# Kernel tuning notes

Measured on AMD Instinct MI355X. Metric: run time of the kernel, lower is better.

Reference implementation:

```python
import jax, jax.numpy as jnp
import numpy as np

NUM_CLASSES = 8
INNER = 2048
BETA = 1.0


def _pairwise_dist(x):
    # ||x_i - x_j||_2 via Gram identity; safe sqrt so grads are finite on the zero diagonal.
    sq = jnp.sum(x * x, axis=-1)
    d2 = jnp.maximum(sq[:, None] + sq[None, :] - 2.0 * (x @ x.T), 0.0)
    safe = jnp.where(d2 > 0, d2, 1.0)
    return jnp.where(d2 > 0, jnp.sqrt(safe), 0.0)


def _mst_edges(dist):
    # Prim's algorithm on a dense [n, n] distance matrix -> (n-1) MST edges.
    # These edges are exactly the death times of 0d persistent homology features.
    n = dist.shape[0]
    big = jnp.finfo(dist.dtype).max
    in_tree = jnp.zeros((n,), bool).at[0].set(True)
    mind = dist[0]                      # best distance from tree to each vertex
    parent = jnp.zeros((n,), jnp.int32)  # tree vertex realizing that distance

    def step(carry, _):
        in_tree, mind, parent = carry
        j = jnp.argmin(jnp.where(in_tree, big, mind)).astype(jnp.int32)
        edge = (parent[j], j)
        in_tree = in_tree.at[j].set(True)
        dj = dist[j]
        upd = dj < mind
        mind = jnp.where(upd, dj, mind)
        parent = jnp.where(upd, j, parent)
        return (in_tree, mind, parent), edge

    _, (e0, e1) = jax.lax.scan(step, (in_tree, mind, parent), None, length=n - 1)
    return e0, e1


def setup_inputs() -> dict:
    key = jax.random.key(0)
    features = jax.random.normal(key, (NUM_CLASSES * INNER, 64), dtype=jnp.float32)
    return {"features": features}


def reference(features):
    feats = features.reshape(NUM_CLASSES, INNER, -1)  # per-class slices

    def per_class(x):
        dist = _pairwise_dist(x)
        e0, e1 = _mst_edges(jax.lax.stop_gradient(dist))  # edge selection has zero gradient
        edge_len = dist[e0, e1]                            # gather MST edge lengths
        return jnp.mean(jnp.abs(edge_len - BETA))          # mean_absolute_error vs beta

    return jnp.sum(jax.vmap(per_class)(feats))  # loss accumulated over classes
```

## Files before the change

### kernel.cpp

```cpp
#include <hip/hip_runtime.h>

#define NCLS 8
#define NPT  2048
#define DIM  64
#define NROUNDS 11
#define NBLK 512
#define CBLK 64
#define FINF 3.402823466e38f
#define INFK 0xFFFFFFFFu
#define INF64 0xFFFFFFFFFFFFFFFFull

#define CTR_FIN      256
#define CTR_FALLBACK 257
#define NCNT         (CTR_FALLBACK + NROUNDS * NCLS)

typedef unsigned int u32;
typedef unsigned long long u64;
typedef unsigned short u16;
typedef _Float16 f16_t;
typedef __attribute__((ext_vector_type(8))) f16_t f16x8;
typedef __attribute__((ext_vector_type(4))) float f32x4;
typedef __attribute__((ext_vector_type(4))) u32 u32x4;

#define MFMAH(a, b, c) __builtin_amdgcn_mfma_f32_16x16x32_f16((a), (b), (c), 0, 0, 0)

#define ALOAD_U64(p) __hip_atomic_load((p), __ATOMIC_RELAXED, __HIP_MEMORY_SCOPE_AGENT)
#define ALOAD_U32(p) __hip_atomic_load((p), __ATOMIC_RELAXED, __HIP_MEMORY_SCOPE_AGENT)
#define ALOAD_F32(p) __hip_atomic_load((p), __ATOMIC_RELAXED, __HIP_MEMORY_SCOPE_AGENT)
#define ASTORE_F32(p, v) __hip_atomic_store((p), (v), __ATOMIC_RELAXED, __HIP_MEMORY_SCOPE_AGENT)

__device__ __forceinline__ void cbar(u32* __restrict__ ctr, int c, int inst) {
    __syncthreads();
    if (threadIdx.x == 0) {
        u32* a = &ctr[c * 32 + inst];
        __hip_atomic_fetch_add(a, 1u, __ATOMIC_RELAXED, __HIP_MEMORY_SCOPE_AGENT);
        while (ALOAD_U32(a) < CBLK) __builtin_amdgcn_s_sleep(1);
    }
    __syncthreads();
}

__global__ void convinit_kernel(const float* __restrict__ x, u16* __restrict__ xh,
                                float* __restrict__ sq, u32* __restrict__ comp,
                                u64* __restrict__ minEdge, float* __restrict__ lossAcc,
                                u32* __restrict__ done, u32* __restrict__ counters) {
    int row  = blockIdx.x * 4 + (threadIdx.x >> 6);
    int lane = threadIdx.x & 63;
    size_t idx = (size_t)row * DIM + lane;
    float v = x[idx];
    xh[idx] = __builtin_bit_cast(u16, (f16_t)v);
    float s = v * v;
    #pragma unroll
    for (int m = 32; m >= 1; m >>= 1) s += __shfl_xor(s, m);
    if (lane == 0) {
        sq[row]   = s;
        comp[row] = (u32)(row & (NPT - 1));
        if (row < NCLS) { lossAcc[row] = 0.0f; done[row] = 0u; }
    }
    int g = blockIdx.x * 256 + threadIdx.x;
    if (g < 2 * NCLS * NPT) minEdge[g] = INF64;
    if (g < NCNT) counters[g] = 0u;
}

__global__ __launch_bounds__(256) void persist2_kernel(
    const u16* __restrict__ xh, const float* __restrict__ sq,
    u64* __restrict__ minEdge, float* __restrict__ lossAcc,
    u32* __restrict__ counters, float* __restrict__ out)
{
    __shared__ u16   compL[NPT];
    __shared__ float sqC[512];
    __shared__ __align__(16) char uni[NPT * 8 + NPT * 2];
    __shared__ float rwS[4];
    __shared__ u32   rcS[4];
    __shared__ u32   shRoot, shConv;

    u64* minT    = (u64*)uni;
    u64* edgeL   = (u64*)uni;
    u16* parentL = (u16*)(uni + NPT * 8);

    const int c    = blockIdx.z;
    const int rb   = blockIdx.y;
    const int cs   = blockIdx.x;
    const int tid  = threadIdx.x;
    const int lane = tid & 63;
    const int w    = tid >> 6;
    const bool leader = (rb == 0 && cs == 0);

    const size_t xbase = (size_t)c * NPT * DIM;
    sqC[tid]       = sq[(size_t)c * NPT + cs * 512 + tid];
    sqC[tid + 256] = sq[(size_t)c * NPT + cs * 512 + 256 + tid];
    #pragma unroll
    for (int k = 0; k < 8; ++k) compL[k * 256 + tid] = (u16)(k * 256 + tid);

    const int kq   = (lane >> 4) * 8;
    const int arow = rb * 128 + w * 32 + (lane & 15);
    f16x8 Ah[2][2];
    #pragma unroll
    for (int rt = 0; rt < 2; ++rt)
        #pragma unroll
        for (int kk = 0; kk < 2; ++kk) {
            size_t off = xbase + (size_t)(arow + rt * 16) * DIM + kk * 32 + kq;
            Ah[rt][kk] = __builtin_bit_cast(f16x8, *(const u32x4*)(xh + off));
        }
    int   rowg_[2][4];
    float sqrow[2][4];
    #pragma unroll
    for (int rt = 0; rt < 2; ++rt)
        #pragma unroll
        for (int r = 0; r < 4; ++r) {
            int rg = rb * 128 + w * 32 + rt * 16 + ((lane >> 4) << 2) + r;
            rowg_[rt][r] = rg;
            sqrow[rt][r] = sq[(size_t)c * NPT + rg];
        }

    float classLoss = 0.0f;
    __syncthreads();

    for (int rnd = 0; rnd < NROUNDS; ++rnd) {
        u64* edgeGb = minEdge + ((size_t)(rnd & 1) * NCLS + c) * NPT;

        #pragma unroll
        for (int k = 0; k < 8; ++k) minT[k * 256 + tid] = INF64;
        __syncthreads();

        u32 crow[2][4];
        #pragma unroll
        for (int rt = 0; rt < 2; ++rt)
            #pragma unroll
            for (int r = 0; r < 4; ++r) crow[rt][r] = compL[rowg_[rt][r]];

        u32 rm[2][4];
        #pragma unroll
        for (int rt = 0; rt < 2; ++rt)
            #pragma unroll
            for (int r = 0; r < 4; ++r) rm[rt][r] = INFK;

        #pragma unroll 2
        for (int ct = 0; ct < 32; ++ct) {
            const int colb = cs * 512 + ct * 16 + (lane & 15);
            f16x8 Bh[2];
            #pragma unroll
            for (int kk = 0; kk < 2; ++kk) {
                size_t off = xbase + (size_t)colb * DIM + kk * 32 + kq;
                Bh[kk] = __builtin_bit_cast(f16x8, *(const u32x4*)(xh + off));
            }
            u32   ccol = compL[colb];
            float sqc_ = sqC[ct * 16 + (lane & 15)];

            #pragma unroll
            for (int rt = 0; rt < 2; ++rt) {
                f32x4 acc = {0.f, 0.f, 0.f, 0.f};
                acc = MFMAH(Ah[rt][0], Bh[0], acc);
                acc = MFMAH(Ah[rt][1], Bh[1], acc);
                #pragma unroll
                for (int r = 0; r < 4; ++r) {
                    float d2 = fmaf(-2.0f, acc[r], sqrow[rt][r] + sqc_);
                    d2 = fmaxf(d2, 0.0f);
                    u32 bk = (__float_as_uint(d2) + 0x400u) & 0xFFFFF800u;
                    u32 k2 = bk | (u32)colb;
                    k2 = (crow[rt][r] == ccol) ? INFK : k2;
                    rm[rt][r] = min(rm[rt][r], k2);
                }
            }
        }

        const u64 tagbits = (u64)(15 - rnd) << 60;
        #pragma unroll
        for (int rt = 0; rt < 2; ++rt)
            #pragma unroll
            for (int r = 0; r < 4; ++r) {
                u32 bv = rm[rt][r];
                #pragma unroll
                for (int m = 8; m >= 1; m >>= 1)
                    bv = min(bv, (u32)__shfl_xor((int)bv, m));
                if ((lane & 15) == 0 && bv != INFK) {
                    int rowg = rowg_[rt][r];
                    int colg = (int)(bv & 0x7FFu);
                    u32 d21  = bv >> 11;
                    int mn = rowg < colg ? rowg : colg;
                    int mx = rowg < colg ? colg : rowg;
                    u64 key = tagbits | ((u64)d21 << 22) | ((u64)mn << 11) | (u64)mx;
                    atomicMin(&minT[crow[rt][r]], key);
                }
            }
        __syncthreads();

        #pragma unroll
        for (int k = 0; k < 8; ++k) {
            int i = k * 256 + tid;
            u64 e = minT[i];
            if (e != INF64) atomicMin(&edgeGb[i], e);
        }

        cbar(counters, c, rnd);

        #pragma unroll
        for (int k = 0; k < 8; ++k) {
            int i = k * 256 + tid;
            edgeL[i]   = ALOAD_U64(&edgeGb[i]);
            parentL[i] = (u16)i;
        }
        __syncthreads();

        const u64 T = (u64)(15 - rnd);
        float myw = 0.0f;
        u32   mycnt = 0;
        #pragma unroll
        for (int k = 0; k < 8; ++k) {
            int L = k * 256 + tid;
            u64 e = edgeL[L];
            if (e != INF64 && (e >> 60) == T) {
                int mn = (int)((e >> 11) & 0x7FF);
                int mx = (int)(e & 0x7FF);
                u32 A = compL[mn], B = compL[mx];
                u32 O = (A == (u32)L) ? B : A;
                bool mutual = (edgeL[O] == e);
                if (!(mutual && (u32)L > O)) {
                    parentL[L] = (u16)O;
                    float d2 = __uint_as_float(((u32)(e >> 22) & 0x1FFFFFu) << 11);
                    myw += fabsf(sqrtf(d2) - 1.0f);
                    ++mycnt;
                }
            }
        }
        __syncthreads();

        #pragma unroll
        for (int k = 0; k < 8; ++k) {
            int L = k * 256 + tid;
            u32 p1 = parentL[L];
            if (p1 != (u32)L && parentL[p1] == (u32)L && (u32)L > p1)
                parentL[L] = (u16)L;
        }
        __syncthreads();

        for (int it = 0; it < 11; ++it) {
            u16 np[8];
            #pragma unroll
            for (int k = 0; k < 8; ++k) {
                int L = k * 256 + tid;
                np[k] = parentL[parentL[L]];
            }
            __syncthreads();
            #pragma unroll
            for (int k = 0; k < 8; ++k) parentL[k * 256 + tid] = np[k];
            __syncthreads();
        }

        u16 nc[8];
        #pragma unroll
        for (int k = 0; k < 8; ++k) nc[k] = parentL[compL[k * 256 + tid]];
        if (tid == 0) { shRoot = nc[0]; shConv = 1; }
        __syncthreads();
        u32 bad = 0;
        #pragma unroll
        for (int k = 0; k < 8; ++k) {
            compL[k * 256 + tid] = nc[k];
            bad |= (u32)(nc[k] != (u16)shRoot);
        }
        if (bad) shConv = 0;

        #pragma unroll
        for (int m = 32; m >= 1; m >>= 1) {
            myw   += __shfl_xor(myw, m);
            mycnt += (u32)__shfl_xor((int)mycnt, m);
        }
        if (lane == 0) { rwS[w] = myw; rcS[w] = mycnt; }
        __syncthreads();

        classLoss += rwS[0] + rwS[1] + rwS[2] + rwS[3];
        u32 rcTot  = rcS[0] + rcS[1] + rcS[2] + rcS[3];
        if (shConv != 0u || rcTot == 0u) break;
    }

    if (leader && tid == 0) ASTORE_F32(&lossAcc[c], classLoss);
    __syncthreads();
    if (leader && tid == 0) {
        u32 t = __hip_atomic_fetch_add(&counters[CTR_FIN], 1u,
                                       __ATOMIC_RELAXED, __HIP_MEMORY_SCOPE_AGENT);
        if (t == NCLS - 1) {
            float s = 0.0f;
            for (int cc = 0; cc < NCLS; ++cc) s += ALOAD_F32(&lossAcc[cc]);
            out[0] = s * (1.0f / (float)(NPT - 1));
        }
    }
}

__global__ __launch_bounds__(256) void scanmerge_kernel(
    const u16* __restrict__ xh, const float* __restrict__ sq,
    u32* __restrict__ comp, u64* __restrict__ minEdge,
    float* __restrict__ lossAcc, u32* __restrict__ classDone,
    u32* __restrict__ counters, int rnd)
{
    const int c = blockIdx.z;
    if (classDone[c]) return;
    const int cs   = blockIdx.x;
    const int rb   = blockIdx.y;
    const int tid  = threadIdx.x;
    const int lane = tid & 63;
    const int w    = tid >> 6;

    __shared__ u32 compL[NPT];
    __shared__ __align__(16) char bufA[NPT * 4];
    __shared__ __align__(16) char bufB[NPT * 8];
    __shared__ float rw[256];
    __shared__ u32   rc[256];
    __shared__ u32   shTicket;
    __shared__ int   conv;

    float* sqL  = (float*)bufA;
    u64*   minT = (u64*)bufB;

    const u32*   compG = comp + (size_t)c * NPT;
    const float* sqG   = sq + (size_t)c * NPT;
    u64*         edgeG = minEdge + (size_t)c * NPT;

    #pragma unroll
    for (int k = 0; k < NPT / 256; ++k) {
        int i = k * 256 + tid;
        compL[i] = compG[i];
        sqL[i]   = sqG[i];
        minT[i]  = INF64;
    }
    __syncthreads();

    const size_t xbase = (size_t)c * NPT * DIM;
    const int    kq    = (lane >> 4) * 8;
    const int    arow  = rb * 128 + w * 32 + (lane & 15);

    f16x8 Ah[2][2];
    #pragma unroll
    for (int rt = 0; rt < 2; ++rt)
        #pragma unroll
        for (int kk = 0; kk < 2; ++kk) {
            size_t off = xbase + (size_t)(arow + rt * 16) * DIM + kk * 32 + kq;
            Ah[rt][kk] = __builtin_bit_cast(f16x8, *(const u32x4*)(xh + off));
        }

    int   rowg_[2][4];
    float sqrow[2][4];
    u32   crow[2][4];
    #pragma unroll
    for (int rt = 0; rt < 2; ++rt)
        #pragma unroll
        for (int r = 0; r < 4; ++r) {
            int rg = rb * 128 + w * 32 + rt * 16 + ((lane >> 4) << 2) + r;
            rowg_[rt][r] = rg;
            sqrow[rt][r] = sqL[rg];
            crow[rt][r]  = compL[rg];
        }

    u32 rm[2][4];
    #pragma unroll
    for (int rt = 0; rt < 2; ++rt)
        #pragma unroll
        for (int r = 0; r < 4; ++r) rm[rt][r] = INFK;

    #pragma unroll 2
    for (int ct = 0; ct < 32; ++ct) {
        const int colb = cs * 512 + ct * 16 + (lane & 15);
        f16x8 Bh[2];
        #pragma unroll
        for (int kk = 0; kk < 2; ++kk) {
            size_t off = xbase + (size_t)colb * DIM + kk * 32 + kq;
            Bh[kk] = __builtin_bit_cast(f16x8, *(const u32x4*)(xh + off));
        }
        u32   ccol = compL[colb];
        float sqc_ = sqL[colb];

        #pragma unroll
        for (int rt = 0; rt < 2; ++rt) {
            f32x4 acc = {0.f, 0.f, 0.f, 0.f};
            acc = MFMAH(Ah[rt][0], Bh[0], acc);
            acc = MFMAH(Ah[rt][1], Bh[1], acc);
            #pragma unroll
            for (int r = 0; r < 4; ++r) {
                float d2 = fmaf(-2.0f, acc[r], sqrow[rt][r] + sqc_);
                d2 = fmaxf(d2, 0.0f);
                u32 bk = (__float_as_uint(d2) + 0x400u) & 0xFFFFF800u;
                u32 k2 = bk | (u32)colb;
                k2 = (crow[rt][r] == ccol) ? INFK : k2;
                rm[rt][r] = min(rm[rt][r], k2);
            }
        }
    }

    #pragma unroll
    for (int rt = 0; rt < 2; ++rt)
        #pragma unroll
        for (int r = 0; r < 4; ++r) {
            u32 bv = rm[rt][r];
            #pragma unroll
            for (int m = 8; m >= 1; m >>= 1)
                bv = min(bv, (u32)__shfl_xor((int)bv, m));
            if ((lane & 15) == 0 && bv != INFK) {
                int rowg = rowg_[rt][r];
                int colg = (int)(bv & 0x7FFu);
                u32 d21  = bv >> 11;
                int mn = rowg < colg ? rowg : colg;
                int mx = rowg < colg ? colg : rowg;
                u64 key = ((u64)d21 << 22) | ((u64)mn << 11) | (u64)mx;
                atomicMin(&minT[crow[rt][r]], key);
            }
        }
    __syncthreads();

    #pragma unroll
    for (int k = 0; k < NPT / 256; ++k) {
        int i = k * 256 + tid;
        u64 e = minT[i];
        if (e != INF64) atomicMin(&edgeG[i], e);
    }

    __syncthreads();
    if (tid == 0)
        shTicket = __hip_atomic_fetch_add(&counters[CTR_FALLBACK + rnd * NCLS + c], 1u,
                                          __ATOMIC_RELAXED, __HIP_MEMORY_SCOPE_AGENT);
    __syncthreads();
    if (shTicket != 63u) return;

    u32* parentL = (u32*)bufA;
    u64* edgeL   = (u64*)bufB;
    u32* compGm  = comp + (size_t)c * NPT;

    #pragma unroll
    for (int k = 0; k < NPT / 256; ++k) {
        int i = k * 256 + tid;
        edgeL[i]   = ALOAD_U64(&edgeG[i]);
        parentL[i] = (u32)i;
    }
    if (tid == 0) conv = 1;
    __syncthreads();

    float myw = 0.0f;
    int   mycnt = 0;
    #pragma unroll
    for (int k = 0; k < NPT / 256; ++k) {
        int L = k * 256 + tid;
        u64 e = edgeL[L];
        if (e != INF64) {
            int mn = (int)((e >> 11) & 0x7FF);
            int mx = (int)(e & 0x7FF);
            u32 A = compL[mn], B = compL[mx];
            u32 O = (A == (u32)L) ? B : A;
            bool mutual = (edgeL[O] == e);
            if (!(mutual && (u32)L > O)) {
                parentL[L] = O;
                float d2 = __uint_as_float((u32)(e >> 22) << 11);
                myw += fabsf(sqrtf(d2) - 1.0f);
                mycnt += 1;
            }
        }
    }
    __syncthreads();

    #pragma unroll
    for (int k = 0; k < NPT / 256; ++k) {
        int L = k * 256 + tid;
        u32 p1 = parentL[L];
        if (p1 != (u32)L && parentL[p1] == (u32)L && (u32)L > p1) parentL[L] = (u32)L;
    }
    __syncthreads();

    for (int it = 0; it < 11; ++it) {
        u32 np[NPT / 256];
        #pragma unroll
        for (int k = 0; k < NPT / 256; ++k) {
            int L = k * 256 + tid;
            np[k] = parentL[parentL[L]];
        }
        __syncthreads();
        #pragma unroll
        for (int k = 0; k < NPT / 256; ++k) parentL[k * 256 + tid] = np[k];
        __syncthreads();
    }

    u32 root0 = parentL[compL[0]];
    #pragma unroll
    for (int k = 0; k < NPT / 256; ++k) {
        int v = k * 256 + tid;
        u32 nc = parentL[compL[v]];
        compGm[v] = nc;
        if (nc != root0) conv = 0;
        edgeG[v] = INF64;
    }

    rw[tid] = myw; rc[tid] = (u32)mycnt;
    __syncthreads();
    for (int s = 128; s >= 1; s >>= 1) {
        if (tid < s) { rw[tid] += rw[tid + s]; rc[tid] += rc[tid + s]; }
        __syncthreads();
    }
    if (tid == 0) {
        lossAcc[c] += rw[0];
        if (conv || rc[0] == 0u) classDone[c] = 1u;
    }
}

__global__ void final2_kernel(const float* __restrict__ lossAcc, float* __restrict__ out) {
    if (threadIdx.x == 0 && blockIdx.x == 0) {
        float s = 0.0f;
        for (int cc = 0; cc < NCLS; ++cc) s += lossAcc[cc] * (1.0f / (float)(NPT - 1));
        out[0] = s;
    }
}

extern "C" void kernel_launch(void* const* d_in, const int* in_sizes, int n_in,
                              void* d_out, int out_size, void* d_ws, size_t ws_size,
                              hipStream_t stream) {
    const float* x   = (const float*)d_in[0];
    float*       out = (float*)d_out;

    const size_t nv = (size_t)NCLS * NPT;
    const size_t nx = (size_t)NCLS * NPT * DIM;

    const size_t off_me   = 0;
    const size_t off_sq   = off_me + 2 * nv * sizeof(u64);
    const size_t off_comp = off_sq + nv * sizeof(float);
    const size_t off_loss = off_comp + nv * sizeof(u32);
    const size_t off_done = off_loss + NCLS * sizeof(float);
    const size_t off_cnt  = off_done + NCLS * sizeof(u32);
    const size_t off_xh   = off_cnt + (((size_t)NCNT + 7) & ~7ull) * sizeof(u32);
    const size_t need     = off_xh + nx * sizeof(u16);

    if (ws_size < need) return;

    u64*   minEdge  = (u64*)((char*)d_ws + off_me);
    float* sq       = (float*)((char*)d_ws + off_sq);
    u32*   comp     = (u32*)((char*)d_ws + off_comp);
    float* lossAcc  = (float*)((char*)d_ws + off_loss);
    u32*   done     = (u32*)((char*)d_ws + off_done);
    u32*   counters = (u32*)((char*)d_ws + off_cnt);
    u16*   xh       = (u16*)((char*)d_ws + off_xh);

    convinit_kernel<<<(NCLS * NPT) / 4, 256, 0, stream>>>(x, xh, sq, comp,
                                                          minEdge, lossAcc, done,
                                                          counters);

    int dev = 0, cus = 0, maxBlk = 0;
    bool coopOK = (hipGetDevice(&dev) == hipSuccess) &&
                  (hipDeviceGetAttribute(&cus, hipDeviceAttributeMultiprocessorCount,
                                         dev) == hipSuccess) &&
                  (hipOccupancyMaxActiveBlocksPerMultiprocessor(
                       &maxBlk, persist2_kernel, 256, 0) == hipSuccess) &&
                  ((long long)maxBlk * cus >= (long long)NBLK);

    if (coopOK) {
        void* args[] = {(void*)&xh, (void*)&sq, (void*)&minEdge,
                        (void*)&lossAcc, (void*)&counters, (void*)&out};
        hipLaunchCooperativeKernel(reinterpret_cast<void*>(persist2_kernel),
                                   dim3(4, 16, NCLS), dim3(256), args, 0, stream);
    } else {
        for (int r = 0; r < NROUNDS; ++r) {
            scanmerge_kernel<<<dim3(4, NPT / 128, NCLS), 256, 0, stream>>>(
                xh, sq, comp, minEdge, lossAcc, done, counters, r);
        }
        final2_kernel<<<1, 64, 0, stream>>>(lossAcc, out);
    }
}
```

Baseline: 136.1 us.

## Use 512-thread blocks with half the grid and early-exit pointer jumping

The persistent Boruvka kernel now runs with 512-thread blocks covering 256 rows each, which halves the grid to 256 blocks. That means fewer participants in the cross-block barrier and fewer global atomic merges of per-block minima. The pointer-jumping loop now tracks whether any parent changed and exits early once converged, and parentL is widened to u32. The trade is fewer resident blocks relative to CUs, so less parallelism in the distance/MFMA phase, plus an extra barrier per jump iteration for the change flag.

```diff
diff --git a/kernel.cpp b/kernel.cpp
--- a/kernel.cpp
+++ b/kernel.cpp
@@ -4,8 +4,8 @@
 #define NPT  2048
 #define DIM  64
 #define NROUNDS 11
-#define NBLK 512
-#define CBLK 64
+#define NBLK 256
+#define CBLK 32
 #define FINF 3.402823466e38f
 #define INFK 0xFFFFFFFFu
 #define INF64 0xFFFFFFFFFFFFFFFFull
@@ -61,21 +61,21 @@
     if (g < NCNT) counters[g] = 0u;
 }
 
-__global__ __launch_bounds__(256) void persist2_kernel(
+__global__ __launch_bounds__(512) void persist3_kernel(
     const u16* __restrict__ xh, const float* __restrict__ sq,
     u64* __restrict__ minEdge, float* __restrict__ lossAcc,
     u32* __restrict__ counters, float* __restrict__ out)
 {
     __shared__ u16   compL[NPT];
     __shared__ float sqC[512];
-    __shared__ __align__(16) char uni[NPT * 8 + NPT * 2];
-    __shared__ float rwS[4];
-    __shared__ u32   rcS[4];
-    __shared__ u32   shRoot, shConv;
-
-    u64* minT    = (u64*)uni;
-    u64* edgeL   = (u64*)uni;
-    u16* parentL = (u16*)(uni + NPT * 8);
+    __shared__ __align__(16) char uni[NPT * 8];
+    __shared__ u32   parentL[NPT];
+    __shared__ float rwS[8];
+    __shared__ u32   rcS[8];
+    __shared__ u32   shRoot, shConv, shChg;
+
+    u64* minT  = (u64*)uni;
+    u64* edgeL = (u64*)uni;
 
     const int c    = blockIdx.z;
     const int rb   = blockIdx.y;
@@ -86,13 +86,12 @@
     const bool leader = (rb == 0 && cs == 0);
 
     const size_t xbase = (size_t)c * NPT * DIM;
-    sqC[tid]       = sq[(size_t)c * NPT + cs * 512 + tid];
-    sqC[tid + 256] = sq[(size_t)c * NPT + cs * 512 + 256 + tid];
-    #pragma unroll
-    for (int k = 0; k < 8; ++k) compL[k * 256 + tid] = (u16)(k * 256 + tid);
+    sqC[tid & 511] = sq[(size_t)c * NPT + cs * 512 + (tid & 511)];
+    #pragma unroll
+    for (int k = 0; k < 4; ++k) compL[k * 512 + tid] = (u16)(k * 512 + tid);
 
     const int kq   = (lane >> 4) * 8;
-    const int arow = rb * 128 + w * 32 + (lane & 15);
+    const int arow = rb * 256 + w * 32 + (lane & 15);
     f16x8 Ah[2][2];
     #pragma unroll
     for (int rt = 0; rt < 2; ++rt)
@@ -107,7 +106,7 @@
     for (int rt = 0; rt < 2; ++rt)
         #pragma unroll
         for (int r = 0; r < 4; ++r) {
-            int rg = rb * 128 + w * 32 + rt * 16 + ((lane >> 4) << 2) + r;
+            int rg = rb * 256 + w * 32 + rt * 16 + ((lane >> 4) << 2) + r;
             rowg_[rt][r] = rg;
             sqrow[rt][r] = sq[(size_t)c * NPT + rg];
         }
@@ -119,7 +118,7 @@
         u64* edgeGb = minEdge + ((size_t)(rnd & 1) * NCLS + c) * NPT;
 
         #pragma unroll
-        for (int k = 0; k < 8; ++k) minT[k * 256 + tid] = INF64;
+        for (int k = 0; k < 4; ++k) minT[k * 512 + tid] = INF64;
         __syncthreads();
 
         u32 crow[2][4];
@@ -134,7 +133,7 @@
             #pragma unroll
             for (int r = 0; r < 4; ++r) rm[rt][r] = INFK;
 
-        #pragma unroll 2
+        #pragma unroll 4
         for (int ct = 0; ct < 32; ++ct) {
             const int colb = cs * 512 + ct * 16 + (lane & 15);
             f16x8 Bh[2];
@@ -185,8 +184,8 @@
         __syncthreads();
 
         #pragma unroll
-        for (int k = 0; k < 8; ++k) {
-            int i = k * 256 + tid;
+        for (int k = 0; k < 4; ++k) {
+            int i = k * 512 + tid;
             u64 e = minT[i];
             if (e != INF64) atomicMin(&edgeGb[i], e);
         }
@@ -194,10 +193,10 @@
         cbar(counters, c, rnd);
 
         #pragma unroll
-        for (int k = 0; k < 8; ++k) {
-            int i = k * 256 + tid;
+        for (int k = 0; k < 4; ++k) {
+            int i = k * 512 + tid;
             edgeL[i]   = ALOAD_U64(&edgeGb[i]);
-            parentL[i] = (u16)i;
+            parentL[i] = (u32)i;
         }
         __syncthreads();
 
@@ -205,8 +204,8 @@
         float myw = 0.0f;
         u32   mycnt = 0;
         #pragma unroll
-        for (int k = 0; k < 8; ++k) {
-            int L = k * 256 + tid;
+        for (int k = 0; k < 4; ++k) {
+            int L = k * 512 + tid;
             u64 e = edgeL[L];
             if (e != INF64 && (e >> 60) == T) {
                 int mn = (int)((e >> 11) & 0x7FF);
@@ -215,7 +214,7 @@
                 u32 O = (A == (u32)L) ? B : A;
                 bool mutual = (edgeL[O] == e);
                 if (!(mutual && (u32)L > O)) {
-                    parentL[L] = (u16)O;
+                    parentL[L] = O;
                     float d2 = __uint_as_float(((u32)(e >> 22) & 0x1FFFFFu) << 11);
                     myw += fabsf(sqrtf(d2) - 1.0f);
                     ++mycnt;
@@ -225,36 +224,42 @@
         __syncthreads();
 
         #pragma unroll
-        for (int k = 0; k < 8; ++k) {
-            int L = k * 256 + tid;
+        for (int k = 0; k < 4; ++k) {
+            int L = k * 512 + tid;
             u32 p1 = parentL[L];
             if (p1 != (u32)L && parentL[p1] == (u32)L && (u32)L > p1)
-                parentL[L] = (u16)L;
-        }
-        __syncthreads();
-
-        for (int it = 0; it < 11; ++it) {
-            u16 np[8];
-            #pragma unroll
-            for (int k = 0; k < 8; ++k) {
-                int L = k * 256 + tid;
-                np[k] = parentL[parentL[L]];
-            }
+                parentL[L] = (u32)L;
+        }
+        __syncthreads();
+
+        for (int itj = 0; itj < 12; ++itj) {
+            if (tid == 0) shChg = 0u;
             __syncthreads();
-            #pragma unroll
-            for (int k = 0; k < 8; ++k) parentL[k * 256 + tid] = np[k];
+            u32 np[4]; u32 ch = 0;
+            #pragma unroll
+            for (int k = 0; k < 4; ++k) {
+                u32 p  = parentL[k * 512 + tid];
+                u32 pp = parentL[p];
+                np[k] = pp;
+                ch |= (u32)(pp != p);
+            }
+            if (ch) shChg = 1u;
             __syncthreads();
-        }
-
-        u16 nc[8];
-        #pragma unroll
-        for (int k = 0; k < 8; ++k) nc[k] = parentL[compL[k * 256 + tid]];
+            if (shChg == 0u) break;
+            #pragma unroll
+            for (int k = 0; k < 4; ++k) parentL[k * 512 + tid] = np[k];
+            __syncthreads();
+        }
+
+        u16 nc[4];
+        #pragma unroll
+        for (int k = 0; k < 4; ++k) nc[k] = (u16)parentL[compL[k * 512 + tid]];
         if (tid == 0) { shRoot = nc[0]; shConv = 1; }
         __syncthreads();
         u32 bad = 0;
         #pragma unroll
-        for (int k = 0; k < 8; ++k) {
-            compL[k * 256 + tid] = nc[k];
+        for (int k = 0; k < 4; ++k) {
+            compL[k * 512 + tid] = nc[k];
             bad |= (u32)(nc[k] != (u16)shRoot);
         }
         if (bad) shConv = 0;
@@ -267,8 +272,10 @@
         if (lane == 0) { rwS[w] = myw; rcS[w] = mycnt; }
         __syncthreads();
 
-        classLoss += rwS[0] + rwS[1] + rwS[2] + rwS[3];
-        u32 rcTot  = rcS[0] + rcS[1] + rcS[2] + rcS[3];
+        float rwTot = 0.0f; u32 rcTot = 0u;
+        #pragma unroll
+        for (int i = 0; i < 8; ++i) { rwTot += rwS[i]; rcTot += rcS[i]; }
+        classLoss += rwTot;
         if (shConv != 0u || rcTot == 0u) break;
     }
 
@@ -541,14 +548,14 @@
                   (hipDeviceGetAttribute(&cus, hipDeviceAttributeMultiprocessorCount,
                                          dev) == hipSuccess) &&
                   (hipOccupancyMaxActiveBlocksPerMultiprocessor(
-                       &maxBlk, persist2_kernel, 256, 0) == hipSuccess) &&
+                       &maxBlk, persist3_kernel, 512, 0) == hipSuccess) &&
                   ((long long)maxBlk * cus >= (long long)NBLK);
 
     if (coopOK) {
         void* args[] = {(void*)&xh, (void*)&sq, (void*)&minEdge,
                         (void*)&lossAcc, (void*)&counters, (void*)&out};
-        hipLaunchCooperativeKernel(reinterpret_cast<void*>(persist2_kernel),
-                                   dim3(4, 16, NCLS), dim3(256), args, 0, stream);
+        hipLaunchCooperativeKernel(reinterpret_cast<void*>(persist3_kernel),
+                                   dim3(4, 8, NCLS), dim3(512), args, 0, stream);
     } else {
         for (int r = 0; r < NROUNDS; ++r) {
             scanmerge_kernel<<<dim3(4, NPT / 128, NCLS), 256, 0, stream>>>(
```

After: 116.7 us. 1.17x faster.
